# Optimization experiments

Measured on AMD Instinct MI355X. Metric: run time of the kernel, lower is better.

## Reference

```python
import jax, jax.numpy as jnp
import numpy as np

D = 1024
H = 16
DH = D // H
NEG = -10000000.0


def setup_inputs() -> dict:
    key = jax.random.key(0)
    ks = jax.random.split(key, 12)
    B, L = 2, 2048
    sc = 0.02
    inp = {
        "q": jax.random.normal(ks[0], (B, L, D), jnp.float32),
        "k": jax.random.normal(ks[1], (B, L, D), jnp.float32),
        "v": jax.random.normal(ks[2], (B, L, D), jnp.float32),
        "attention_mask": jax.random.randint(ks[3], (B, L, L), 0, 2) == 1,
        "head_mask": jnp.ones((1, 1, 1), jnp.float32),
        "Wq": sc * jax.random.normal(ks[4], (D, D), jnp.float32),
        "bq": jnp.zeros((D,), jnp.float32),
        "Wk": sc * jax.random.normal(ks[5], (D, D), jnp.float32),
        "bk": jnp.zeros((D,), jnp.float32),
        "Wv": sc * jax.random.normal(ks[6], (D, D), jnp.float32),
        "bv": jnp.zeros((D,), jnp.float32),
        "Wo": sc * jax.random.normal(ks[7], (D, D), jnp.float32),
        "bo": jnp.zeros((D,), jnp.float32),
    }
    return inp


def reference(q, k, v, attention_mask, head_mask, Wq, bq, Wk, bk, Wv, bv, Wo, bo):
    B, Lq, _ = q.shape
    Lk = k.shape[1]
    # QKV projections (nn.Linear: x @ W.T + b), split into heads
    qh = (q @ Wq.T + bq).reshape(B, Lq, H, DH)  # [B,Lq,H,dh]
    kh = (k @ Wk.T + bk).reshape(B, Lk, H, DH)
    vh = (v @ Wv.T + bv).reshape(B, Lk, H, DH)
    # scores [B,H,Lq,Lk], scaled by 1/sqrt(dh)
    scores = jnp.einsum("bihd,bjhd->bhij", qh, kh) / jnp.sqrt(jnp.float32(DH))
    scores = jnp.where(attention_mask[:, None, :, :], NEG, scores)
    probs = jax.nn.softmax(scores, axis=-1)
    probs = probs * head_mask  # broadcastable head mask (dropout is identity in eval)
    ctx = jnp.einsum("bhij,bjhd->bihd", probs, vh).reshape(B, Lq, D)
    # output linear + residual (Add_and_LN with with_lN=False, eval dropout)
    out = ctx @ Wo.T + bo + q
    return out
```

## Files before the change

kernel.cpp:

```cpp
#include <hip/hip_runtime.h>

typedef unsigned short u16;
typedef unsigned long long u64;
typedef __attribute__((ext_vector_type(4))) float f32x4;
typedef __attribute__((ext_vector_type(8))) short s16x8;
typedef __attribute__((ext_vector_type(4))) short s16x4;
typedef __attribute__((ext_vector_type(4))) unsigned int u32x4;

#define LDS_LOAD16(gp, lp) __builtin_amdgcn_global_load_lds( \
    (__attribute__((address_space(1))) void*)(gp), \
    (__attribute__((address_space(3))) void*)(lp), 16, 0, 0)

#define MFMA16 __builtin_amdgcn_mfma_f32_16x16x32_bf16

constexpr float L2E = 1.44269504088896340736f;

__device__ __forceinline__ u16 f2bf(float x) {
  unsigned u = __float_as_uint(x);
  u += 0x7FFF + ((u >> 16) & 1);
  return (u16)(u >> 16);
}

__device__ __forceinline__ unsigned cvtpk_bf16(float lo, float hi) {
  unsigned r;
  asm("v_cvt_pk_bf16_f32 %0, %1, %2" : "=v"(r) : "v"(lo), "v"(hi));
  return r;
}

struct PrepArgs {
  const float* src[7];
  u16* dst[7];
  int n4[7];
  float scale[7];
  const unsigned* mask;
  u64* bits;
  int nmask;
  int nconv;
};

__global__ __launch_bounds__(256) void prep_all(PrepArgs a) {
  const int arr = blockIdx.y;
  if (arr == a.nconv) {
    const int lane = threadIdx.x & 63;
    unsigned probe = a.mask[lane];
    bool bytemode = __any(probe > 1u);
    const int stride = gridDim.x * blockDim.x;
    for (int i = blockIdx.x * blockDim.x + threadIdx.x; i < a.nmask; i += stride) {
      bool v;
      if (bytemode) v = ((const unsigned char*)a.mask)[i] != 0;
      else          v = a.mask[i] != 0;
      u64 b = __ballot(v);
      if (lane == 0) a.bits[i >> 6] = b;
    }
    return;
  }
  const f32x4* src = (const f32x4*)a.src[arr];
  u16* dst = a.dst[arr];
  const int n4 = a.n4[arr];
  const float sc = a.scale[arr];
  const int stride = gridDim.x * blockDim.x;
  for (int i = blockIdx.x * blockDim.x + threadIdx.x; i < n4; i += stride) {
    f32x4 v = src[i];
    s16x4 o;
#pragma unroll
    for (int j = 0; j < 4; ++j) o[j] = (short)f2bf(v[j] * sc);
    *(s16x4*)(dst + (size_t)i * 4) = o;
  }
}

struct QkvArgsB {
  const u16* A[3];
  const u16* B[3];
  const float* bias[3];
  float bscale[3];
  u16* C[3];
};

__global__ __launch_bounds__(256) void gemm_qkv_bf(QkvArgsB a) {
  const int z = blockIdx.z;
  const u16* __restrict__ A = a.A[z];
  const u16* __restrict__ B = a.B[z];
  const float* __restrict__ bias = a.bias[z];
  const float bscale = a.bscale[z];
  u16* __restrict__ C = a.C[z];

  __shared__ u16 As[3][4096];
  __shared__ u16 Bs[3][4096];
  const int tid = threadIdx.x;
  const int lane = tid & 63;
  const int wave = tid >> 6;
  const int g = lane >> 4, c = lane & 15;
  const int g4 = g * 4;
  const int bx = blockIdx.x;
  const int row0 = (((bx & 7) << 2) | (bx >> 3)) * 128;
  const int col0 = blockIdx.y * 128;
  const int wr = (wave >> 1) * 64, wc = (wave & 1) * 64;

  f32x4 acc[4][4] = {};

#define STAGE_QKV(p_, k0_) { _Pragma("unroll") \
    for (int i = 0; i < 2; ++i) { \
      int e = (i * 256 + tid) * 8; \
      LDS_LOAD16(A + (size_t)(row0 + (e >> 5)) * 1024 + (k0_) + (e & 31), As[p_] + e); \
      LDS_LOAD16(B + (size_t)(col0 + (e >> 5)) * 1024 + (k0_) + (e & 31), Bs[p_] + e); } }

  STAGE_QKV(0, 0);
  STAGE_QKV(1, 32);

  for (int s = 0; s < 32; ++s) {
    const int p = s % 3;
    if (s == 31) asm volatile("s_waitcnt vmcnt(0)" ::: "memory");
    else         asm volatile("s_waitcnt vmcnt(4)" ::: "memory");
    __builtin_amdgcn_s_barrier();
    __builtin_amdgcn_sched_barrier(0);
    if (s + 2 < 32) {
      const int np = (s + 2) % 3;
      STAGE_QKV(np, (s + 2) * 32);
    }
    s16x8 af[4], bf[4];
#pragma unroll
    for (int m = 0; m < 4; ++m) af[m] = *(const s16x8*)(As[p] + (wr + m * 16 + c) * 32 + g * 8);
#pragma unroll
    for (int n = 0; n < 4; ++n) bf[n] = *(const s16x8*)(Bs[p] + (wc + n * 16 + c) * 32 + g * 8);
#pragma unroll
    for (int m = 0; m < 4; ++m)
#pragma unroll
      for (int n = 0; n < 4; ++n)
        acc[m][n] = MFMA16(bf[n], af[m], acc[m][n], 0, 0, 0);
  }

  f32x4 bv[4];
#pragma unroll
  for (int n = 0; n < 4; ++n) {
    bv[n] = *(const f32x4*)(bias + col0 + wc + n * 16 + g4);
#pragma unroll
    for (int r = 0; r < 4; ++r) bv[n][r] *= bscale;
  }
#pragma unroll
  for (int m = 0; m < 4; ++m)
#pragma unroll
    for (int n = 0; n < 4; ++n) {
      s16x4 o;
#pragma unroll
      for (int r = 0; r < 4; ++r) o[r] = (short)f2bf(acc[m][n][r] + bv[n][r]);
      *(s16x4*)(C + (size_t)(row0 + wr + m * 16 + c) * 1024 + col0 + wc + n * 16 + g4) = o;
    }
}

struct QkvArgsF {
  const float* A[3];
  const u16* B[3];
  const float* bias[3];
  float bscale[3];
  u16* C[3];
};

__global__ __launch_bounds__(256) void gemm_qkv_f32(QkvArgsF a) {
  const int z = blockIdx.z;
  const float* __restrict__ A = a.A[z];
  const u16* __restrict__ B = a.B[z];
  const float* __restrict__ bias = a.bias[z];
  const float bscale = a.bscale[z];
  u16* __restrict__ C = a.C[z];

  __shared__ u16 As[2][4096];
  __shared__ u16 Bs[2][4096];
  const int tid = threadIdx.x;
  const int lane = tid & 63;
  const int wave = tid >> 6;
  const int g = lane >> 4, c = lane & 15;
  const int g4 = g * 4;
  const int row0 = blockIdx.x * 128;
  const int col0 = blockIdx.y * 128;
  const int wr = (wave >> 1) * 64, wc = (wave & 1) * 64;
  const int ra = tid >> 2;
  const int cca = (tid & 3) * 8;

  f32x4 acc[4][4] = {};
  f32x4 ar[2][2];
#pragma unroll
  for (int i = 0; i < 2; ++i) {
    ar[i][0] = *(const f32x4*)(A + (size_t)(row0 + i * 64 + ra) * 1024 + cca);
    ar[i][1] = *(const f32x4*)(A + (size_t)(row0 + i * 64 + ra) * 1024 + cca + 4);
  }

  for (int s = 0; s < 32; ++s) {
    const int p = s & 1;
    const int k0 = s * 32;
#pragma unroll
    for (int i = 0; i < 2; ++i) {
      unsigned w0 = cvtpk_bf16(ar[i][0][0], ar[i][0][1]);
      unsigned w1 = cvtpk_bf16(ar[i][0][2], ar[i][0][3]);
      unsigned w2 = cvtpk_bf16(ar[i][1][0], ar[i][1][1]);
      unsigned w3 = cvtpk_bf16(ar[i][1][2], ar[i][1][3]);
      union { u32x4 u; s16x8 v; } w;
      w.u = (u32x4){w0, w1, w2, w3};
      *(s16x8*)(As[p] + (i * 256 + tid) * 8) = w.v;
    }
    if (s < 31) {
#pragma unroll
      for (int i = 0; i < 2; ++i) {
        ar[i][0] = *(const f32x4*)(A + (size_t)(row0 + i * 64 + ra) * 1024 + k0 + 32 + cca);
        ar[i][1] = *(const f32x4*)(A + (size_t)(row0 + i * 64 + ra) * 1024 + k0 + 32 + cca + 4);
      }
    }
#pragma unroll
    for (int i = 0; i < 2; ++i) {
      int e = (i * 256 + tid) * 8;
      LDS_LOAD16(B + (size_t)(col0 + (e >> 5)) * 1024 + k0 + (e & 31), Bs[p] + e);
    }
    __syncthreads();

    s16x8 af[4], bf[4];
#pragma unroll
    for (int m = 0; m < 4; ++m) af[m] = *(const s16x8*)(As[p] + (wr + m * 16 + c) * 32 + g * 8);
#pragma unroll
    for (int n = 0; n < 4; ++n) bf[n] = *(const s16x8*)(Bs[p] + (wc + n * 16 + c) * 32 + g * 8);
#pragma unroll
    for (int m = 0; m < 4; ++m)
#pragma unroll
      for (int n = 0; n < 4; ++n)
        acc[m][n] = MFMA16(bf[n], af[m], acc[m][n], 0, 0, 0);
  }

  f32x4 bv[4];
#pragma unroll
  for (int n = 0; n < 4; ++n) {
    bv[n] = *(const f32x4*)(bias + col0 + wc + n * 16 + g4);
#pragma unroll
    for (int r = 0; r < 4; ++r) bv[n][r] *= bscale;
  }
#pragma unroll
  for (int m = 0; m < 4; ++m)
#pragma unroll
    for (int n = 0; n < 4; ++n) {
      s16x4 o;
#pragma unroll
      for (int r = 0; r < 4; ++r) o[r] = (short)f2bf(acc[m][n][r] + bv[n][r]);
      *(s16x4*)(C + (size_t)(row0 + wr + m * 16 + c) * 1024 + col0 + wc + n * 16 + g4) = o;
    }
}

__global__ __launch_bounds__(256) void gemm_out(const u16* __restrict__ A,
                                                const u16* __restrict__ B,
                                                const float* __restrict__ bias,
                                                const float* __restrict__ resid,
                                                float* __restrict__ C) {
  __shared__ u16 As[3][2048];
  __shared__ u16 Bs[3][4096];
  const int tid = threadIdx.x;
  const int lane = tid & 63;
  const int wave = tid >> 6;
  const int g = lane >> 4, c = lane & 15;
  const int g4 = g * 4;
  const int bx = blockIdx.x;
  const int row0 = (((bx & 7) << 3) | (bx >> 3)) * 64;
  const int col0 = blockIdx.y * 128;
  const int wr = (wave >> 1) * 32, wc = (wave & 1) * 64;

  f32x4 acc[2][4] = {};

#define STAGE_OUT(p_, k0_) { \
    LDS_LOAD16(A + (size_t)(row0 + (tid >> 2)) * 1024 + (k0_) + (tid & 3) * 8, As[p_] + tid * 8); \
    _Pragma("unroll") \
    for (int i = 0; i < 2; ++i) { \
      int e = (i * 256 + tid) * 8; \
      LDS_LOAD16(B + (size_t)(col0 + (e >> 5)) * 1024 + (k0_) + (e & 31), Bs[p_] + e); } }

  STAGE_OUT(0, 0);
  STAGE_OUT(1, 32);

  for (int s = 0; s < 32; ++s) {
    const int p = s % 3;
    if (s == 31) asm volatile("s_waitcnt vmcnt(0)" ::: "memory");
    else         asm volatile("s_waitcnt vmcnt(3)" ::: "memory");
    __builtin_amdgcn_s_barrier();
    __builtin_amdgcn_sched_barrier(0);
    if (s + 2 < 32) {
      const int np = (s + 2) % 3;
      STAGE_OUT(np, (s + 2) * 32);
    }
    s16x8 af[2], bf[4];
#pragma unroll
    for (int m = 0; m < 2; ++m) af[m] = *(const s16x8*)(As[p] + (wr + m * 16 + c) * 32 + g * 8);
#pragma unroll
    for (int n = 0; n < 4; ++n) bf[n] = *(const s16x8*)(Bs[p] + (wc + n * 16 + c) * 32 + g * 8);
#pragma unroll
    for (int m = 0; m < 2; ++m)
#pragma unroll
      for (int n = 0; n < 4; ++n)
        acc[m][n] = MFMA16(bf[n], af[m], acc[m][n], 0, 0, 0);
  }

  f32x4 bv[4];
#pragma unroll
  for (int n = 0; n < 4; ++n) bv[n] = *(const f32x4*)(bias + col0 + wc + n * 16 + g4);
#pragma unroll
  for (int m = 0; m < 2; ++m)
#pragma unroll
    for (int n = 0; n < 4; ++n) {
      size_t off = (size_t)(row0 + wr + m * 16 + c) * 1024 + col0 + wc + n * 16 + g4;
      f32x4 rv = *(const f32x4*)(resid + off);
      f32x4 o;
#pragma unroll
      for (int r = 0; r < 4; ++r) o[r] = acc[m][n][r] + bv[n][r] + rv[r];
      *(f32x4*)(C + off) = o;
    }
}

constexpr float NEGV = -10000000.0f;

__global__ __launch_bounds__(256) void attn_kernel(const u16* __restrict__ Qh,
                                                   const u16* __restrict__ Kh,
                                                   const u16* __restrict__ Vh,
                                                   const u64* __restrict__ mbits,
                                                   const float* __restrict__ head_mask,
                                                   u16* __restrict__ ctx) {
  __shared__ u16 Ks[2][4096];
  __shared__ u16 Vt[2][64 * 72];

  const int tid = threadIdx.x;
  const int lane = tid & 63;
  const int wave = tid >> 6;
  const int g = lane >> 4, c = lane & 15;
  const int g4 = g * 4;
  const int wid = (blockIdx.x & 7) * 64 + (blockIdx.x >> 3);
  const int qt = wid & 15;
  const int bh = wid >> 4;
  const int b = bh >> 4;
  const int h = bh & 15;
  const size_t rowbase = (size_t)b * 2048;
  const int D = 1024;

  s16x8 qf[2][2];
#pragma unroll
  for (int s = 0; s < 2; ++s) {
    const int qrow = qt * 128 + s * 64 + wave * 16 + c;
#pragma unroll
    for (int ks = 0; ks < 2; ++ks)
      qf[s][ks] = *(const s16x8*)(Qh + (rowbase + qrow) * D + h * 64 + ks * 32 + g * 8);
  }

  f32x4 accO[2][4] = {};
  f32x4 accSum[2] = {};

  union { u32x4 u; s16x8 v; } onesu;
  onesu.u = (u32x4){0x3F803F80u, 0x3F803F80u, 0x3F803F80u, 0x3F803F80u};
  const s16x8 onesA = onesu.v;

  const u64* mrow0 = mbits + (rowbase + qt * 128 + 0 * 64 + wave * 16 + c) * 32;
  const u64* mrow1 = mbits + (rowbase + qt * 128 + 1 * 64 + wave * 16 + c) * 32;

  const int kkK = tid & 63;
  const int aV = tid >> 3;
  const int sV = tid & 7;
  const int dcV = sV * 8;
  const int k2 = 2 * aV;
  const int slotV = (k2 & 32) | (((k2 >> 2) & 3) << 3) | (((k2 >> 4) & 1) << 2) | (k2 & 3);
  const int colV = slotV ^ (8 * sV);

  const u16* Kbase = Kh + rowbase * D + h * 64;
  const u16* Vbase = Vh + rowbase * D + h * 64;

  s16x8 kreg[2], vreg[2];
#define LOADKV(kb_) { \
    kreg[0] = *(const s16x8*)(Kbase + (size_t)((kb_) + kkK) * D + wave * 8); \
    kreg[1] = *(const s16x8*)(Kbase + (size_t)((kb_) + kkK) * D + (4 + wave) * 8); \
    vreg[0] = *(const s16x8*)(Vbase + (size_t)((kb_) + k2) * D + dcV); \
    vreg[1] = *(const s16x8*)(Vbase + (size_t)((kb_) + k2 + 1) * D + dcV); }
#define WRITEKV(p_) { \
    *(s16x8*)(Ks[p_] + tid * 8) = kreg[0]; \
    *(s16x8*)(Ks[p_] + 2048 + tid * 8) = kreg[1]; \
    const unsigned* v0w = (const unsigned*)&vreg[0]; \
    const unsigned* v1w = (const unsigned*)&vreg[1]; \
    _Pragma("unroll") \
    for (int j = 0; j < 8; ++j) { \
      unsigned pk = __builtin_amdgcn_perm(v1w[j >> 1], v0w[j >> 1], \
                                          (j & 1) ? 0x07060302u : 0x05040100u); \
      *(unsigned*)(Vt[p_] + (dcV + j) * 72 + colV) = pk; } }

  LOADKV(0);
  WRITEKV(0);
  LOADKV(64);
  __syncthreads();

#define ATTN_ITER(p_, it_) { \
    const int it = (it_); \
    if (it < 31) WRITEKV(p_ ^ 1); \
    if (it < 30) LOADKV((it + 2) * 64); \
    f32x4 accS[2][4]; \
    _Pragma("unroll") \
    for (int t = 0; t < 4; ++t) { \
      s16x8 kf0 = *(const s16x8*)(Ks[p_] + ((0 + g) * 64 + t * 16 + c) * 8); \
      s16x8 kf1 = *(const s16x8*)(Ks[p_] + ((4 + g) * 64 + t * 16 + c) * 8); \
      f32x4 z0 = {0.f, 0.f, 0.f, 0.f}; \
      z0 = MFMA16(kf0, qf[0][0], z0, 0, 0, 0); \
      accS[0][t] = MFMA16(kf1, qf[0][1], z0, 0, 0, 0); \
      f32x4 z1 = {0.f, 0.f, 0.f, 0.f}; \
      z1 = MFMA16(kf0, qf[1][0], z1, 0, 0, 0); \
      accS[1][t] = MFMA16(kf1, qf[1][1], z1, 0, 0, 0); \
    } \
    s16x8 vbr[4][2]; \
    _Pragma("unroll") \
    for (int d0 = 0; d0 < 4; ++d0) { \
      const int dd = d0 * 16 + c; \
      const int sw8 = (d0 * 2 + (c >> 3)) * 8; \
      _Pragma("unroll") \
      for (int ks = 0; ks < 2; ++ks) \
        vbr[d0][ks] = *(const s16x8*)(Vt[p_] + dd * 72 + ((ks * 32 + g * 8) ^ sw8)); \
    } \
    s16x8 pa[2][2]; \
    _Pragma("unroll") \
    for (int s = 0; s < 2; ++s) { \
      u64 mw = (s == 0 ? mrow0 : mrow1)[it]; \
      u64 sh = mw >> g4; \
      unsigned mlo = (unsigned)sh, mhi = (unsigned)(sh >> 32); \
      unsigned pk0[4], pk1[4]; \
      _Pragma("unroll") \
      for (int t = 0; t < 4; ++t) { \
        unsigned msrc = (t < 2) ? mlo : mhi; \
        _Pragma("unroll") \
        for (int r = 0; r < 4; ++r) { \
          float sv = accS[s][t][r]; \
          if ((msrc >> ((t & 1) * 16 + r)) & 1) sv = NEGV; \
          float pv; \
          asm("v_exp_f32 %0, %1" : "=v"(pv) : "v"(sv)); \
          accS[s][t][r] = pv; \
        } \
        pk0[t] = cvtpk_bf16(accS[s][t][0], accS[s][t][1]); \
        pk1[t] = cvtpk_bf16(accS[s][t][2], accS[s][t][3]); \
      } \
      _Pragma("unroll") \
      for (int ks = 0; ks < 2; ++ks) { \
        union { u32x4 u; s16x8 v; } w; \
        w.u = (u32x4){pk0[2 * ks], pk1[2 * ks], pk0[2 * ks + 1], pk1[2 * ks + 1]}; \
        pa[s][ks] = w.v; \
      } \
    } \
    _Pragma("unroll") \
    for (int d0 = 0; d0 < 4; ++d0) \
      _Pragma("unroll") \
      for (int ks = 0; ks < 2; ++ks) { \
        accO[0][d0] = MFMA16(vbr[d0][ks], pa[0][ks], accO[0][d0], 0, 0, 0); \
        accO[1][d0] = MFMA16(vbr[d0][ks], pa[1][ks], accO[1][d0], 0, 0, 0); \
      } \
    _Pragma("unroll") \
    for (int ks = 0; ks < 2; ++ks) { \
      accSum[0] = MFMA16(onesA, pa[0][ks], accSum[0], 0, 0, 0); \
      accSum[1] = MFMA16(onesA, pa[1][ks], accSum[1], 0, 0, 0); \
    } \
    __syncthreads(); }

  for (int it2 = 0; it2 < 16; ++it2) {
    ATTN_ITER(0, 2 * it2);
    ATTN_ITER(1, 2 * it2 + 1);
  }

  const float hm = head_mask[0];
#pragma unroll
  for (int s = 0; s < 2; ++s) {
    float inv = hm / accSum[s][0];
    const int qrow = qt * 128 + s * 64 + wave * 16 + c;
#pragma unroll
    for (int d0 = 0; d0 < 4; ++d0) {
      s16x4 o;
#pragma unroll
      for (int r = 0; r < 4; ++r) o[r] = (short)f2bf(accO[s][d0][r] * inv);
      *(s16x4*)(ctx + (rowbase + qrow) * D + h * 64 + d0 * 16 + g4) = o;
    }
  }
}

extern "C" void kernel_launch(void* const* d_in, const int* in_sizes, int n_in,
                              void* d_out, int out_size, void* d_ws, size_t ws_size,
                              hipStream_t stream) {
  const float* q  = (const float*)d_in[0];
  const float* k  = (const float*)d_in[1];
  const float* v  = (const float*)d_in[2];
  const void*  am = d_in[3];
  const float* hm = (const float*)d_in[4];
  const float* Wq = (const float*)d_in[5];
  const float* bq = (const float*)d_in[6];
  const float* Wk = (const float*)d_in[7];
  const float* bk = (const float*)d_in[8];
  const float* Wv = (const float*)d_in[9];
  const float* bv = (const float*)d_in[10];
  const float* Wo = (const float*)d_in[11];
  const float* bo = (const float*)d_in[12];

  char* ws = (char*)d_ws;
  const size_t MB = 1024 * 1024;
  const bool big = ws_size >= 58 * MB;

  if (big) {
    u16* qb  = (u16*)(ws + 0 * MB);
    u16* kb  = (u16*)(ws + 8 * MB);
    u16* vb  = (u16*)(ws + 16 * MB);
    u16* wqb = (u16*)(ws + 24 * MB);
    u16* wkb = (u16*)(ws + 26 * MB);
    u16* wvb = (u16*)(ws + 28 * MB);
    u16* wob = (u16*)(ws + 30 * MB);
    u16* Qh  = (u16*)(ws + 32 * MB);
    u16* Kh  = (u16*)(ws + 40 * MB);
    u16* Vh  = (u16*)(ws + 48 * MB);
    u64* mbits = (u64*)(ws + 56 * MB);
    u16* ctx = qb;

    PrepArgs ca;
    ca.src[0] = q;  ca.dst[0] = qb;  ca.n4[0] = 1048576; ca.scale[0] = 1.f;
    ca.src[1] = k;  ca.dst[1] = kb;  ca.n4[1] = 1048576; ca.scale[1] = 1.f;
    ca.src[2] = v;  ca.dst[2] = vb;  ca.n4[2] = 1048576; ca.scale[2] = 1.f;
    ca.src[3] = Wq; ca.dst[3] = wqb; ca.n4[3] = 262144;  ca.scale[3] = 0.125f * L2E;
    ca.src[4] = Wk; ca.dst[4] = wkb; ca.n4[4] = 262144;  ca.scale[4] = 1.f;
    ca.src[5] = Wv; ca.dst[5] = wvb; ca.n4[5] = 262144;  ca.scale[5] = 1.f;
    ca.src[6] = Wo; ca.dst[6] = wob; ca.n4[6] = 262144;  ca.scale[6] = 1.f;
    ca.mask = (const unsigned*)am; ca.bits = mbits; ca.nmask = 8388608; ca.nconv = 7;
    prep_all<<<dim3(512, 8), 256, 0, stream>>>(ca);

    QkvArgsB ga;
    ga.A[0] = qb; ga.B[0] = wqb; ga.bias[0] = bq; ga.bscale[0] = 0.125f * L2E; ga.C[0] = Qh;
    ga.A[1] = kb; ga.B[1] = wkb; ga.bias[1] = bk; ga.bscale[1] = 1.f;          ga.C[1] = Kh;
    ga.A[2] = vb; ga.B[2] = wvb; ga.bias[2] = bv; ga.bscale[2] = 1.f;          ga.C[2] = Vh;
    gemm_qkv_bf<<<dim3(32, 8, 3), 256, 0, stream>>>(ga);

    attn_kernel<<<512, 256, 0, stream>>>(Qh, Kh, Vh, mbits, hm, ctx);

    gemm_out<<<dim3(64, 8), 256, 0, stream>>>(ctx, wob, bo, q, (float*)d_out);
  } else {
    u16* Qh  = (u16*)(ws + 0 * MB);
    u16* Kh  = (u16*)(ws + 8 * MB);
    u16* Vh  = (u16*)(ws + 16 * MB);
    u16* wqb = (u16*)(ws + 24 * MB);
    u16* wkb = (u16*)(ws + 26 * MB);
    u16* wvb = (u16*)(ws + 28 * MB);
    u16* wob = (u16*)(ws + 30 * MB);
    u64* mbits = (u64*)(ws + 32 * MB);
    u16* ctx = (u16*)(ws + 33 * MB);

    PrepArgs ca;
    ca.src[0] = Wq; ca.dst[0] = wqb; ca.n4[0] = 262144; ca.scale[0] = 0.125f * L2E;
    ca.src[1] = Wk; ca.dst[1] = wkb; ca.n4[1] = 262144; ca.scale[1] = 1.f;
    ca.src[2] = Wv; ca.dst[2] = wvb; ca.n4[2] = 262144; ca.scale[2] = 1.f;
    ca.src[3] = Wo; ca.dst[3] = wob; ca.n4[3] = 262144; ca.scale[3] = 1.f;
    ca.mask = (const unsigned*)am; ca.bits = mbits; ca.nmask = 8388608; ca.nconv = 4;
    prep_all<<<dim3(512, 5), 256, 0, stream>>>(ca);

    QkvArgsF ga;
    ga.A[0] = q; ga.B[0] = wqb; ga.bias[0] = bq; ga.bscale[0] = 0.125f * L2E; ga.C[0] = Qh;
    ga.A[1] = k; ga.B[1] = wkb; ga.bias[1] = bk; ga.bscale[1] = 1.f;          ga.C[1] = Kh;
    ga.A[2] = v; ga.B[2] = wvb; ga.bias[2] = bv; ga.bscale[2] = 1.f;          ga.C[2] = Vh;
    gemm_qkv_f32<<<dim3(32, 8, 3), 256, 0, stream>>>(ga);

    attn_kernel<<<512, 256, 0, stream>>>(Qh, Kh, Vh, mbits, hm, ctx);

    gemm_out<<<dim3(64, 8), 256, 0, stream>>>(ctx, wob, bo, q, (float*)d_out);
  }
}
```

Measured before the change: 164.9 us.

## Halve attention query tile to 64 rows and split mask prep kernel

The attention kernel now gives each block 64 query rows instead of 128, doubling the grid to 1024 blocks and adding a launch-bounds hint of 4 blocks per CU for occupancy. Fewer accumulators per thread lowers register pressure, but each K/V tile loaded into LDS is now reused by half as many queries, so K/V traffic doubles. The mask-to-bitmask conversion is also split out of the fused prep kernel into its own launch, which adds one kernel launch.

```diff
diff --git a/kernel.cpp b/kernel.cpp
--- a/kernel.cpp
+++ b/kernel.cpp
@@ -27,33 +27,15 @@
   return r;
 }
 
-struct PrepArgs {
+struct ConvArgs {
   const float* src[7];
   u16* dst[7];
   int n4[7];
   float scale[7];
-  const unsigned* mask;
-  u64* bits;
-  int nmask;
-  int nconv;
 };
 
-__global__ __launch_bounds__(256) void prep_all(PrepArgs a) {
+__global__ __launch_bounds__(256) void convert_many(ConvArgs a) {
   const int arr = blockIdx.y;
-  if (arr == a.nconv) {
-    const int lane = threadIdx.x & 63;
-    unsigned probe = a.mask[lane];
-    bool bytemode = __any(probe > 1u);
-    const int stride = gridDim.x * blockDim.x;
-    for (int i = blockIdx.x * blockDim.x + threadIdx.x; i < a.nmask; i += stride) {
-      bool v;
-      if (bytemode) v = ((const unsigned char*)a.mask)[i] != 0;
-      else          v = a.mask[i] != 0;
-      u64 b = __ballot(v);
-      if (lane == 0) a.bits[i >> 6] = b;
-    }
-    return;
-  }
   const f32x4* src = (const f32x4*)a.src[arr];
   u16* dst = a.dst[arr];
   const int n4 = a.n4[arr];
@@ -65,6 +47,22 @@
 #pragma unroll
     for (int j = 0; j < 4; ++j) o[j] = (short)f2bf(v[j] * sc);
     *(s16x4*)(dst + (size_t)i * 4) = o;
+  }
+}
+
+__global__ __launch_bounds__(256) void mask_to_bits(const unsigned int* __restrict__ m32,
+                                                    u64* __restrict__ bits,
+                                                    int n) {
+  const int lane = threadIdx.x & 63;
+  unsigned probe = m32[lane];
+  bool bytemode = __any(probe > 1u);
+  const int stride = gridDim.x * blockDim.x;
+  for (int i = blockIdx.x * blockDim.x + threadIdx.x; i < n; i += stride) {
+    bool v;
+    if (bytemode) v = ((const unsigned char*)m32)[i] != 0;
+    else          v = m32[i] != 0;
+    u64 b = __ballot(v);
+    if (lane == 0) bits[i >> 6] = b;
   }
 }
 
@@ -310,12 +308,12 @@
 
 constexpr float NEGV = -10000000.0f;
 
-__global__ __launch_bounds__(256) void attn_kernel(const u16* __restrict__ Qh,
-                                                   const u16* __restrict__ Kh,
-                                                   const u16* __restrict__ Vh,
-                                                   const u64* __restrict__ mbits,
-                                                   const float* __restrict__ head_mask,
-                                                   u16* __restrict__ ctx) {
+__global__ __launch_bounds__(256, 4) void attn_kernel(const u16* __restrict__ Qh,
+                                                      const u16* __restrict__ Kh,
+                                                      const u16* __restrict__ Vh,
+                                                      const u64* __restrict__ mbits,
+                                                      const float* __restrict__ head_mask,
+                                                      u16* __restrict__ ctx) {
   __shared__ u16 Ks[2][4096];
   __shared__ u16 Vt[2][64 * 72];
 
@@ -324,32 +322,28 @@
   const int wave = tid >> 6;
   const int g = lane >> 4, c = lane & 15;
   const int g4 = g * 4;
-  const int wid = (blockIdx.x & 7) * 64 + (blockIdx.x >> 3);
-  const int qt = wid & 15;
-  const int bh = wid >> 4;
+  const int wid = (blockIdx.x & 7) * 128 + (blockIdx.x >> 3);
+  const int qt = wid & 31;
+  const int bh = wid >> 5;
   const int b = bh >> 4;
   const int h = bh & 15;
   const size_t rowbase = (size_t)b * 2048;
   const int D = 1024;
 
-  s16x8 qf[2][2];
-#pragma unroll
-  for (int s = 0; s < 2; ++s) {
-    const int qrow = qt * 128 + s * 64 + wave * 16 + c;
-#pragma unroll
-    for (int ks = 0; ks < 2; ++ks)
-      qf[s][ks] = *(const s16x8*)(Qh + (rowbase + qrow) * D + h * 64 + ks * 32 + g * 8);
-  }
-
-  f32x4 accO[2][4] = {};
-  f32x4 accSum[2] = {};
+  const int qrow = qt * 64 + wave * 16 + c;
+  s16x8 qf[2];
+#pragma unroll
+  for (int ks = 0; ks < 2; ++ks)
+    qf[ks] = *(const s16x8*)(Qh + (rowbase + qrow) * D + h * 64 + ks * 32 + g * 8);
+
+  f32x4 accO[4] = {};
+  f32x4 accSum = {};
 
   union { u32x4 u; s16x8 v; } onesu;
   onesu.u = (u32x4){0x3F803F80u, 0x3F803F80u, 0x3F803F80u, 0x3F803F80u};
   const s16x8 onesA = onesu.v;
 
-  const u64* mrow0 = mbits + (rowbase + qt * 128 + 0 * 64 + wave * 16 + c) * 32;
-  const u64* mrow1 = mbits + (rowbase + qt * 128 + 1 * 64 + wave * 16 + c) * 32;
+  const u64* mrow = mbits + (rowbase + qrow) * 32;
 
   const int kkK = tid & 63;
   const int aV = tid >> 3;
@@ -388,17 +382,14 @@
     const int it = (it_); \
     if (it < 31) WRITEKV(p_ ^ 1); \
     if (it < 30) LOADKV((it + 2) * 64); \
-    f32x4 accS[2][4]; \
+    f32x4 accS[4]; \
     _Pragma("unroll") \
     for (int t = 0; t < 4; ++t) { \
       s16x8 kf0 = *(const s16x8*)(Ks[p_] + ((0 + g) * 64 + t * 16 + c) * 8); \
       s16x8 kf1 = *(const s16x8*)(Ks[p_] + ((4 + g) * 64 + t * 16 + c) * 8); \
-      f32x4 z0 = {0.f, 0.f, 0.f, 0.f}; \
-      z0 = MFMA16(kf0, qf[0][0], z0, 0, 0, 0); \
-      accS[0][t] = MFMA16(kf1, qf[0][1], z0, 0, 0, 0); \
-      f32x4 z1 = {0.f, 0.f, 0.f, 0.f}; \
-      z1 = MFMA16(kf0, qf[1][0], z1, 0, 0, 0); \
-      accS[1][t] = MFMA16(kf1, qf[1][1], z1, 0, 0, 0); \
+      f32x4 z = {0.f, 0.f, 0.f, 0.f}; \
+      z = MFMA16(kf0, qf[0], z, 0, 0, 0); \
+      accS[t] = MFMA16(kf1, qf[1], z, 0, 0, 0); \
     } \
     s16x8 vbr[4][2]; \
     _Pragma("unroll") \
@@ -409,46 +400,39 @@
       for (int ks = 0; ks < 2; ++ks) \
         vbr[d0][ks] = *(const s16x8*)(Vt[p_] + dd * 72 + ((ks * 32 + g * 8) ^ sw8)); \
     } \
-    s16x8 pa[2][2]; \
-    _Pragma("unroll") \
-    for (int s = 0; s < 2; ++s) { \
-      u64 mw = (s == 0 ? mrow0 : mrow1)[it]; \
-      u64 sh = mw >> g4; \
-      unsigned mlo = (unsigned)sh, mhi = (unsigned)(sh >> 32); \
-      unsigned pk0[4], pk1[4]; \
+    u64 mw = mrow[it]; \
+    u64 sh = mw >> g4; \
+    unsigned mlo = (unsigned)sh, mhi = (unsigned)(sh >> 32); \
+    unsigned pk0[4], pk1[4]; \
+    _Pragma("unroll") \
+    for (int t = 0; t < 4; ++t) { \
+      unsigned msrc = (t < 2) ? mlo : mhi; \
       _Pragma("unroll") \
-      for (int t = 0; t < 4; ++t) { \
-        unsigned msrc = (t < 2) ? mlo : mhi; \
-        _Pragma("unroll") \
-        for (int r = 0; r < 4; ++r) { \
-          float sv = accS[s][t][r]; \
-          if ((msrc >> ((t & 1) * 16 + r)) & 1) sv = NEGV; \
-          float pv; \
-          asm("v_exp_f32 %0, %1" : "=v"(pv) : "v"(sv)); \
-          accS[s][t][r] = pv; \
-        } \
-        pk0[t] = cvtpk_bf16(accS[s][t][0], accS[s][t][1]); \
-        pk1[t] = cvtpk_bf16(accS[s][t][2], accS[s][t][3]); \
+      for (int r = 0; r < 4; ++r) { \
+        float sv = accS[t][r]; \
+        if ((msrc >> ((t & 1) * 16 + r)) & 1) sv = NEGV; \
+        float pv; \
+        asm("v_exp_f32 %0, %1" : "=v"(pv) : "v"(sv)); \
+        accS[t][r] = pv; \
       } \
-      _Pragma("unroll") \
-      for (int ks = 0; ks < 2; ++ks) { \
-        union { u32x4 u; s16x8 v; } w; \
-        w.u = (u32x4){pk0[2 * ks], pk1[2 * ks], pk0[2 * ks + 1], pk1[2 * ks + 1]}; \
-        pa[s][ks] = w.v; \
-      } \
+      pk0[t] = cvtpk_bf16(accS[t][0], accS[t][1]); \
+      pk1[t] = cvtpk_bf16(accS[t][2], accS[t][3]); \
+    } \
+    s16x8 pa[2]; \
+    _Pragma("unroll") \
+    for (int ks = 0; ks < 2; ++ks) { \
+      union { u32x4 u; s16x8 v; } w; \
+      w.u = (u32x4){pk0[2 * ks], pk1[2 * ks], pk0[2 * ks + 1], pk1[2 * ks + 1]}; \
+      pa[ks] = w.v; \
     } \
     _Pragma("unroll") \
     for (int d0 = 0; d0 < 4; ++d0) \
       _Pragma("unroll") \
-      for (int ks = 0; ks < 2; ++ks) { \
-        accO[0][d0] = MFMA16(vbr[d0][ks], pa[0][ks], accO[0][d0], 0, 0, 0); \
-        accO[1][d0] = MFMA16(vbr[d0][ks], pa[1][ks], accO[1][d0], 0, 0, 0); \
-      } \
-    _Pragma("unroll") \
-    for (int ks = 0; ks < 2; ++ks) { \
-      accSum[0] = MFMA16(onesA, pa[0][ks], accSum[0], 0, 0, 0); \
-      accSum[1] = MFMA16(onesA, pa[1][ks], accSum[1], 0, 0, 0); \
-    } \
+      for (int ks = 0; ks < 2; ++ks) \
+        accO[d0] = MFMA16(vbr[d0][ks], pa[ks], accO[d0], 0, 0, 0); \
+    _Pragma("unroll") \
+    for (int ks = 0; ks < 2; ++ks) \
+      accSum = MFMA16(onesA, pa[ks], accSum, 0, 0, 0); \
     __syncthreads(); }
 
   for (int it2 = 0; it2 < 16; ++it2) {
@@ -457,17 +441,13 @@
   }
 
   const float hm = head_mask[0];
-#pragma unroll
-  for (int s = 0; s < 2; ++s) {
-    float inv = hm / accSum[s][0];
-    const int qrow = qt * 128 + s * 64 + wave * 16 + c;
-#pragma unroll
-    for (int d0 = 0; d0 < 4; ++d0) {
-      s16x4 o;
-#pragma unroll
-      for (int r = 0; r < 4; ++r) o[r] = (short)f2bf(accO[s][d0][r] * inv);
-      *(s16x4*)(ctx + (rowbase + qrow) * D + h * 64 + d0 * 16 + g4) = o;
-    }
+  float inv = hm / accSum[0];
+#pragma unroll
+  for (int d0 = 0; d0 < 4; ++d0) {
+    s16x4 o;
+#pragma unroll
+    for (int r = 0; r < 4; ++r) o[r] = (short)f2bf(accO[d0][r] * inv);
+    *(s16x4*)(ctx + (rowbase + qrow) * D + h * 64 + d0 * 16 + g4) = o;
   }
 }
 
@@ -506,7 +486,7 @@
     u64* mbits = (u64*)(ws + 56 * MB);
     u16* ctx = qb;
 
-    PrepArgs ca;
+    ConvArgs ca;
     ca.src[0] = q;  ca.dst[0] = qb;  ca.n4[0] = 1048576; ca.scale[0] = 1.f;
     ca.src[1] = k;  ca.dst[1] = kb;  ca.n4[1] = 1048576; ca.scale[1] = 1.f;
     ca.src[2] = v;  ca.dst[2] = vb;  ca.n4[2] = 1048576; ca.scale[2] = 1.f;
@@ -514,8 +494,9 @@
     ca.src[4] = Wk; ca.dst[4] = wkb; ca.n4[4] = 262144;  ca.scale[4] = 1.f;
     ca.src[5] = Wv; ca.dst[5] = wvb; ca.n4[5] = 262144;  ca.scale[5] = 1.f;
     ca.src[6] = Wo; ca.dst[6] = wob; ca.n4[6] = 262144;  ca.scale[6] = 1.f;
-    ca.mask = (const unsigned*)am; ca.bits = mbits; ca.nmask = 8388608; ca.nconv = 7;
-    prep_all<<<dim3(512, 8), 256, 0, stream>>>(ca);
+    convert_many<<<dim3(512, 7), 256, 0, stream>>>(ca);
+
+    mask_to_bits<<<2048, 256, 0, stream>>>((const unsigned int*)am, mbits, 8388608);
 
     QkvArgsB ga;
     ga.A[0] = qb; ga.B[0] = wqb; ga.bias[0] = bq; ga.bscale[0] = 0.125f * L2E; ga.C[0] = Qh;
@@ -523,7 +504,7 @@
     ga.A[2] = vb; ga.B[2] = wvb; ga.bias[2] = bv; ga.bscale[2] = 1.f;          ga.C[2] = Vh;
     gemm_qkv_bf<<<dim3(32, 8, 3), 256, 0, stream>>>(ga);
 
-    attn_kernel<<<512, 256, 0, stream>>>(Qh, Kh, Vh, mbits, hm, ctx);
+    attn_kernel<<<1024, 256, 0, stream>>>(Qh, Kh, Vh, mbits, hm, ctx);
 
     gemm_out<<<dim3(64, 8), 256, 0, stream>>>(ctx, wob, bo, q, (float*)d_out);
   } else {
@@ -537,13 +518,14 @@
     u64* mbits = (u64*)(ws + 32 * MB);
     u16* ctx = (u16*)(ws + 33 * MB);
 
-    PrepArgs ca;
+    ConvArgs ca;
     ca.src[0] = Wq; ca.dst[0] = wqb; ca.n4[0] = 262144; ca.scale[0] = 0.125f * L2E;
     ca.src[1] = Wk; ca.dst[1] = wkb; ca.n4[1] = 262144; ca.scale[1] = 1.f;
     ca.src[2] = Wv; ca.dst[2] = wvb; ca.n4[2] = 262144; ca.scale[2] = 1.f;
     ca.src[3] = Wo; ca.dst[3] = wob; ca.n4[3] = 262144; ca.scale[3] = 1.f;
-    ca.mask = (const unsigned*)am; ca.bits = mbits; ca.nmask = 8388608; ca.nconv = 4;
-    prep_all<<<dim3(512, 5), 256, 0, stream>>>(ca);
+    convert_many<<<dim3(256, 4), 256, 0, stream>>>(ca);
+
+    mask_to_bits<<<2048, 256, 0, stream>>>((const unsigned int*)am, mbits, 8388608);
 
     QkvArgsF ga;
     ga.A[0] = q; ga.B[0] = wqb; ga.bias[0] = bq; ga.bscale[0] = 0.125f * L2E; ga.C[0] = Qh;
@@ -551,7 +533,7 @@
     ga.A[2] = v; ga.B[2] = wvb; ga.bias[2] = bv; ga.bscale[2] = 1.f;          ga.C[2] = Vh;
     gemm_qkv_f32<<<dim3(32, 8, 3), 256, 0, stream>>>(ga);
 
-    attn_kernel<<<512, 256, 0, stream>>>(Qh, Kh, Vh, mbits, hm, ctx);
+    attn_kernel<<<1024, 256, 0, stream>>>(Qh, Kh, Vh, mbits, hm, ctx);
 
     gemm_out<<<dim3(64, 8), 256, 0, stream>>>(ctx, wob, bo, q, (float*)d_out);
   }
```

After: 151.5 us. 8.1% less time.

## Split attention over key halves with a combine pass; separate mask kernel

Applied to the files above, without the earlier changes.

Attention now runs 1024 blocks, each covering half of the key sequence. Each block writes unnormalized bf16 partial outputs and row sums, and a new combine kernel adds the halves and normalizes. The goal is more parallelism and better CU occupancy, helped by launch_bounds(256,4). The mask-to-bits conversion moves out of the fused prep kernel into its own launch. This costs an extra kernel launch plus a round trip through global memory for the partials, and rounding the partials to bf16 loses some precision.

```diff
diff --git a/kernel.cpp b/kernel.cpp
--- a/kernel.cpp
+++ b/kernel.cpp
@@ -21,39 +21,25 @@
   return (u16)(u >> 16);
 }
 
+__device__ __forceinline__ float bf2f(u16 x) {
+  return __uint_as_float(((unsigned)x) << 16);
+}
+
 __device__ __forceinline__ unsigned cvtpk_bf16(float lo, float hi) {
   unsigned r;
   asm("v_cvt_pk_bf16_f32 %0, %1, %2" : "=v"(r) : "v"(lo), "v"(hi));
   return r;
 }
 
-struct PrepArgs {
+struct ConvArgs {
   const float* src[7];
   u16* dst[7];
   int n4[7];
   float scale[7];
-  const unsigned* mask;
-  u64* bits;
-  int nmask;
-  int nconv;
 };
 
-__global__ __launch_bounds__(256) void prep_all(PrepArgs a) {
+__global__ __launch_bounds__(256) void convert_many(ConvArgs a) {
   const int arr = blockIdx.y;
-  if (arr == a.nconv) {
-    const int lane = threadIdx.x & 63;
-    unsigned probe = a.mask[lane];
-    bool bytemode = __any(probe > 1u);
-    const int stride = gridDim.x * blockDim.x;
-    for (int i = blockIdx.x * blockDim.x + threadIdx.x; i < a.nmask; i += stride) {
-      bool v;
-      if (bytemode) v = ((const unsigned char*)a.mask)[i] != 0;
-      else          v = a.mask[i] != 0;
-      u64 b = __ballot(v);
-      if (lane == 0) a.bits[i >> 6] = b;
-    }
-    return;
-  }
   const f32x4* src = (const f32x4*)a.src[arr];
   u16* dst = a.dst[arr];
   const int n4 = a.n4[arr];
@@ -65,6 +51,22 @@
 #pragma unroll
     for (int j = 0; j < 4; ++j) o[j] = (short)f2bf(v[j] * sc);
     *(s16x4*)(dst + (size_t)i * 4) = o;
+  }
+}
+
+__global__ __launch_bounds__(256) void mask_to_bits(const unsigned int* __restrict__ m32,
+                                                    u64* __restrict__ bits,
+                                                    int n) {
+  const int lane = threadIdx.x & 63;
+  unsigned probe = m32[lane];
+  bool bytemode = __any(probe > 1u);
+  const int stride = gridDim.x * blockDim.x;
+  for (int i = blockIdx.x * blockDim.x + threadIdx.x; i < n; i += stride) {
+    bool v;
+    if (bytemode) v = ((const unsigned char*)m32)[i] != 0;
+    else          v = m32[i] != 0;
+    u64 b = __ballot(v);
+    if (lane == 0) bits[i >> 6] = b;
   }
 }
 
@@ -310,12 +312,16 @@
 
 constexpr float NEGV = -10000000.0f;
 
-__global__ __launch_bounds__(256) void attn_kernel(const u16* __restrict__ Qh,
-                                                   const u16* __restrict__ Kh,
-                                                   const u16* __restrict__ Vh,
-                                                   const u64* __restrict__ mbits,
-                                                   const float* __restrict__ head_mask,
-                                                   u16* __restrict__ ctx) {
+__global__ __launch_bounds__(256, 4) void attn_kernel(const u16* __restrict__ Qh,
+                                                      const u16* __restrict__ Kh,
+                                                      const u16* __restrict__ Vh,
+                                                      const u64* __restrict__ mbits,
+                                                      const float* __restrict__ head_mask,
+                                                      u16* __restrict__ O0,
+                                                      u16* __restrict__ O1,
+                                                      float* __restrict__ s0p,
+                                                      float* __restrict__ s1p,
+                                                      int niter) {
   __shared__ u16 Ks[2][4096];
   __shared__ u16 Vt[2][64 * 72];
 
@@ -324,13 +330,18 @@
   const int wave = tid >> 6;
   const int g = lane >> 4, c = lane & 15;
   const int g4 = g * 4;
-  const int wid = (blockIdx.x & 7) * 64 + (blockIdx.x >> 3);
+  const int nb = gridDim.x >> 3;
+  const int wid = (blockIdx.x & 7) * nb + (blockIdx.x >> 3);
   const int qt = wid & 15;
-  const int bh = wid >> 4;
+  const int rest = wid >> 4;
+  const int bh = rest & 31;
+  const int half = rest >> 5;
   const int b = bh >> 4;
   const int h = bh & 15;
   const size_t rowbase = (size_t)b * 2048;
   const int D = 1024;
+  const int kb0 = half * niter * 64;
+  const int mbase = half * niter;
 
   s16x8 qf[2][2];
 #pragma unroll
@@ -379,15 +390,15 @@
                                           (j & 1) ? 0x07060302u : 0x05040100u); \
       *(unsigned*)(Vt[p_] + (dcV + j) * 72 + colV) = pk; } }
 
-  LOADKV(0);
+  LOADKV(kb0);
   WRITEKV(0);
-  LOADKV(64);
+  LOADKV(kb0 + 64);
   __syncthreads();
 
 #define ATTN_ITER(p_, it_) { \
     const int it = (it_); \
-    if (it < 31) WRITEKV(p_ ^ 1); \
-    if (it < 30) LOADKV((it + 2) * 64); \
+    if (it < niter - 1) WRITEKV(p_ ^ 1); \
+    if (it < niter - 2) LOADKV(kb0 + (it + 2) * 64); \
     f32x4 accS[2][4]; \
     _Pragma("unroll") \
     for (int t = 0; t < 4; ++t) { \
@@ -412,7 +423,7 @@
     s16x8 pa[2][2]; \
     _Pragma("unroll") \
     for (int s = 0; s < 2; ++s) { \
-      u64 mw = (s == 0 ? mrow0 : mrow1)[it]; \
+      u64 mw = (s == 0 ? mrow0 : mrow1)[mbase + it]; \
       u64 sh = mw >> g4; \
       unsigned mlo = (unsigned)sh, mhi = (unsigned)(sh >> 32); \
       unsigned pk0[4], pk1[4]; \
@@ -451,23 +462,65 @@
     } \
     __syncthreads(); }
 
-  for (int it2 = 0; it2 < 16; ++it2) {
+  const int n2 = niter >> 1;
+  for (int it2 = 0; it2 < n2; ++it2) {
     ATTN_ITER(0, 2 * it2);
     ATTN_ITER(1, 2 * it2 + 1);
   }
 
-  const float hm = head_mask[0];
-#pragma unroll
-  for (int s = 0; s < 2; ++s) {
-    float inv = hm / accSum[s][0];
-    const int qrow = qt * 128 + s * 64 + wave * 16 + c;
-#pragma unroll
-    for (int d0 = 0; d0 < 4; ++d0) {
-      s16x4 o;
-#pragma unroll
-      for (int r = 0; r < 4; ++r) o[r] = (short)f2bf(accO[s][d0][r] * inv);
-      *(s16x4*)(ctx + (rowbase + qrow) * D + h * 64 + d0 * 16 + g4) = o;
-    }
+  if (s0p) {
+    u16* outp = half ? O1 : O0;
+    float* sp = half ? s1p : s0p;
+#pragma unroll
+    for (int s = 0; s < 2; ++s) {
+      const int qrow = qt * 128 + s * 64 + wave * 16 + c;
+      if (g == 0) sp[(rowbase + qrow) * 16 + h] = accSum[s][0];
+#pragma unroll
+      for (int d0 = 0; d0 < 4; ++d0) {
+        s16x4 o;
+#pragma unroll
+        for (int r = 0; r < 4; ++r) o[r] = (short)f2bf(accO[s][d0][r]);
+        *(s16x4*)(outp + (rowbase + qrow) * D + h * 64 + d0 * 16 + g4) = o;
+      }
+    }
+  } else {
+    const float hm = head_mask[0];
+#pragma unroll
+    for (int s = 0; s < 2; ++s) {
+      float inv = hm / accSum[s][0];
+      const int qrow = qt * 128 + s * 64 + wave * 16 + c;
+#pragma unroll
+      for (int d0 = 0; d0 < 4; ++d0) {
+        s16x4 o;
+#pragma unroll
+        for (int r = 0; r < 4; ++r) o[r] = (short)f2bf(accO[s][d0][r] * inv);
+        *(s16x4*)(O0 + (rowbase + qrow) * D + h * 64 + d0 * 16 + g4) = o;
+      }
+    }
+  }
+}
+
+__global__ __launch_bounds__(256) void combine_halves(const u16* __restrict__ O0,
+                                                      const u16* __restrict__ O1,
+                                                      const float* __restrict__ s0,
+                                                      const float* __restrict__ s1,
+                                                      const float* __restrict__ hm,
+                                                      u16* __restrict__ ctx) {
+  const float hmv = hm[0];
+  const int stride = gridDim.x * blockDim.x;
+  for (int i = blockIdx.x * blockDim.x + threadIdx.x; i < 524288; i += stride) {
+    const int e = i * 8;
+    const int row = e >> 10;
+    const int h = (e >> 6) & 15;
+    const int sidx = row * 16 + h;
+    const float inv = hmv / (s0[sidx] + s1[sidx]);
+    s16x8 a = *(const s16x8*)(O0 + e);
+    s16x8 bb = *(const s16x8*)(O1 + e);
+    s16x8 o;
+#pragma unroll
+    for (int j = 0; j < 8; ++j)
+      o[j] = (short)f2bf((bf2f((u16)a[j]) + bf2f((u16)bb[j])) * inv);
+    *(s16x8*)(ctx + e) = o;
   }
 }
 
@@ -504,9 +557,11 @@
     u16* Kh  = (u16*)(ws + 40 * MB);
     u16* Vh  = (u16*)(ws + 48 * MB);
     u64* mbits = (u64*)(ws + 56 * MB);
+    float* sums0 = (float*)(ws + 57 * MB);
+    float* sums1 = (float*)(ws + 57 * MB + 262144);
     u16* ctx = qb;
 
-    PrepArgs ca;
+    ConvArgs ca;
     ca.src[0] = q;  ca.dst[0] = qb;  ca.n4[0] = 1048576; ca.scale[0] = 1.f;
     ca.src[1] = k;  ca.dst[1] = kb;  ca.n4[1] = 1048576; ca.scale[1] = 1.f;
     ca.src[2] = v;  ca.dst[2] = vb;  ca.n4[2] = 1048576; ca.scale[2] = 1.f;
@@ -514,8 +569,9 @@
     ca.src[4] = Wk; ca.dst[4] = wkb; ca.n4[4] = 262144;  ca.scale[4] = 1.f;
     ca.src[5] = Wv; ca.dst[5] = wvb; ca.n4[5] = 262144;  ca.scale[5] = 1.f;
     ca.src[6] = Wo; ca.dst[6] = wob; ca.n4[6] = 262144;  ca.scale[6] = 1.f;
-    ca.mask = (const unsigned*)am; ca.bits = mbits; ca.nmask = 8388608; ca.nconv = 7;
-    prep_all<<<dim3(512, 8), 256, 0, stream>>>(ca);
+    convert_many<<<dim3(512, 7), 256, 0, stream>>>(ca);
+
+    mask_to_bits<<<2048, 256, 0, stream>>>((const unsigned int*)am, mbits, 8388608);
 
     QkvArgsB ga;
     ga.A[0] = qb; ga.B[0] = wqb; ga.bias[0] = bq; ga.bscale[0] = 0.125f * L2E; ga.C[0] = Qh;
@@ -523,7 +579,9 @@
     ga.A[2] = vb; ga.B[2] = wvb; ga.bias[2] = bv; ga.bscale[2] = 1.f;          ga.C[2] = Vh;
     gemm_qkv_bf<<<dim3(32, 8, 3), 256, 0, stream>>>(ga);
 
-    attn_kernel<<<512, 256, 0, stream>>>(Qh, Kh, Vh, mbits, hm, ctx);
+    attn_kernel<<<1024, 256, 0, stream>>>(Qh, Kh, Vh, mbits, hm,
+                                          kb, vb, sums0, sums1, 16);
+    combine_halves<<<2048, 256, 0, stream>>>(kb, vb, sums0, sums1, hm, ctx);
 
     gemm_out<<<dim3(64, 8), 256, 0, stream>>>(ctx, wob, bo, q, (float*)d_out);
   } else {
@@ -537,13 +595,14 @@
     u64* mbits = (u64*)(ws + 32 * MB);
     u16* ctx = (u16*)(ws + 33 * MB);
 
-    PrepArgs ca;
+    ConvArgs ca;
     ca.src[0] = Wq; ca.dst[0] = wqb; ca.n4[0] = 262144; ca.scale[0] = 0.125f * L2E;
     ca.src[1] = Wk; ca.dst[1] = wkb; ca.n4[1] = 262144; ca.scale[1] = 1.f;
     ca.src[2] = Wv; ca.dst[2] = wvb; ca.n4[2] = 262144; ca.scale[2] = 1.f;
     ca.src[3] = Wo; ca.dst[3] = wob; ca.n4[3] = 262144; ca.scale[3] = 1.f;
-    ca.mask = (const unsigned*)am; ca.bits = mbits; ca.nmask = 8388608; ca.nconv = 4;
-    prep_all<<<dim3(512, 5), 256, 0, stream>>>(ca);
+    convert_many<<<dim3(256, 4), 256, 0, stream>>>(ca);
+
+    mask_to_bits<<<2048, 256, 0, stream>>>((const unsigned int*)am, mbits, 8388608);
 
     QkvArgsF ga;
     ga.A[0] = q; ga.B[0] = wqb; ga.bias[0] = bq; ga.bscale[0] = 0.125f * L2E; ga.C[0] = Qh;
@@ -551,7 +610,8 @@
     ga.A[2] = v; ga.B[2] = wvb; ga.bias[2] = bv; ga.bscale[2] = 1.f;          ga.C[2] = Vh;
     gemm_qkv_f32<<<dim3(32, 8, 3), 256, 0, stream>>>(ga);
 
-    attn_kernel<<<512, 256, 0, stream>>>(Qh, Kh, Vh, mbits, hm, ctx);
+    attn_kernel<<<512, 256, 0, stream>>>(Qh, Kh, Vh, mbits, hm,
+                                         ctx, nullptr, nullptr, nullptr, 32);
 
     gemm_out<<<dim3(64, 8), 256, 0, stream>>>(ctx, wob, bo, q, (float*)d_out);
   }
```

Result: slower. 176.3 us (+6.9%).

## Move mask bit-packing into QKV GEMM launch to overlap with matmul

Applied to the files above, without the earlier changes.

On the large-workspace path, the attention-mask-to-bitmask conversion moves out of the prep kernel and into an extra z-slice of the QKV GEMM grid. The memory-bound mask pass then runs alongside the compute-bound GEMM blocks instead of beside the conversion work, which is also memory-bound. The small-workspace path splits mask packing into its own kernel launch, which adds a launch there. Risks are an extra slice of 256 blocks in the GEMM grid and weaker overlap if the mask blocks are scheduled last.

```diff
diff --git a/kernel.cpp b/kernel.cpp
--- a/kernel.cpp
+++ b/kernel.cpp
@@ -27,33 +27,15 @@
   return r;
 }
 
-struct PrepArgs {
+struct ConvArgs {
   const float* src[7];
   u16* dst[7];
   int n4[7];
   float scale[7];
-  const unsigned* mask;
-  u64* bits;
-  int nmask;
-  int nconv;
 };
 
-__global__ __launch_bounds__(256) void prep_all(PrepArgs a) {
+__global__ __launch_bounds__(256) void convert_many(ConvArgs a) {
   const int arr = blockIdx.y;
-  if (arr == a.nconv) {
-    const int lane = threadIdx.x & 63;
-    unsigned probe = a.mask[lane];
-    bool bytemode = __any(probe > 1u);
-    const int stride = gridDim.x * blockDim.x;
-    for (int i = blockIdx.x * blockDim.x + threadIdx.x; i < a.nmask; i += stride) {
-      bool v;
-      if (bytemode) v = ((const unsigned char*)a.mask)[i] != 0;
-      else          v = a.mask[i] != 0;
-      u64 b = __ballot(v);
-      if (lane == 0) a.bits[i >> 6] = b;
-    }
-    return;
-  }
   const f32x4* src = (const f32x4*)a.src[arr];
   u16* dst = a.dst[arr];
   const int n4 = a.n4[arr];
@@ -68,16 +50,51 @@
   }
 }
 
+__global__ __launch_bounds__(256) void mask_to_bits(const unsigned int* __restrict__ m32,
+                                                    u64* __restrict__ bits,
+                                                    int n) {
+  const int lane = threadIdx.x & 63;
+  unsigned probe = m32[lane];
+  bool bytemode = __any(probe > 1u);
+  const int stride = gridDim.x * blockDim.x;
+  for (int i = blockIdx.x * blockDim.x + threadIdx.x; i < n; i += stride) {
+    bool v;
+    if (bytemode) v = ((const unsigned char*)m32)[i] != 0;
+    else          v = m32[i] != 0;
+    u64 b = __ballot(v);
+    if (lane == 0) bits[i >> 6] = b;
+  }
+}
+
 struct QkvArgsB {
   const u16* A[3];
   const u16* B[3];
   const float* bias[3];
   float bscale[3];
   u16* C[3];
+  const unsigned* mask;
+  u64* bits;
+  int nmask;
 };
 
 __global__ __launch_bounds__(256) void gemm_qkv_bf(QkvArgsB a) {
   const int z = blockIdx.z;
+  if (z == 3) {
+    const int lane = threadIdx.x & 63;
+    unsigned probe = a.mask[lane];
+    bool bytemode = __any(probe > 1u);
+    const int nb = gridDim.x * gridDim.y;
+    const int bid = blockIdx.y * gridDim.x + blockIdx.x;
+    const int stride = nb * blockDim.x;
+    for (int i = bid * blockDim.x + threadIdx.x; i < a.nmask; i += stride) {
+      bool v;
+      if (bytemode) v = ((const unsigned char*)a.mask)[i] != 0;
+      else          v = a.mask[i] != 0;
+      u64 b = __ballot(v);
+      if (lane == 0) a.bits[i >> 6] = b;
+    }
+    return;
+  }
   const u16* __restrict__ A = a.A[z];
   const u16* __restrict__ B = a.B[z];
   const float* __restrict__ bias = a.bias[z];
@@ -506,7 +523,7 @@
     u64* mbits = (u64*)(ws + 56 * MB);
     u16* ctx = qb;
 
-    PrepArgs ca;
+    ConvArgs ca;
     ca.src[0] = q;  ca.dst[0] = qb;  ca.n4[0] = 1048576; ca.scale[0] = 1.f;
     ca.src[1] = k;  ca.dst[1] = kb;  ca.n4[1] = 1048576; ca.scale[1] = 1.f;
     ca.src[2] = v;  ca.dst[2] = vb;  ca.n4[2] = 1048576; ca.scale[2] = 1.f;
@@ -514,14 +531,14 @@
     ca.src[4] = Wk; ca.dst[4] = wkb; ca.n4[4] = 262144;  ca.scale[4] = 1.f;
     ca.src[5] = Wv; ca.dst[5] = wvb; ca.n4[5] = 262144;  ca.scale[5] = 1.f;
     ca.src[6] = Wo; ca.dst[6] = wob; ca.n4[6] = 262144;  ca.scale[6] = 1.f;
-    ca.mask = (const unsigned*)am; ca.bits = mbits; ca.nmask = 8388608; ca.nconv = 7;
-    prep_all<<<dim3(512, 8), 256, 0, stream>>>(ca);
+    convert_many<<<dim3(512, 7), 256, 0, stream>>>(ca);
 
     QkvArgsB ga;
     ga.A[0] = qb; ga.B[0] = wqb; ga.bias[0] = bq; ga.bscale[0] = 0.125f * L2E; ga.C[0] = Qh;
     ga.A[1] = kb; ga.B[1] = wkb; ga.bias[1] = bk; ga.bscale[1] = 1.f;          ga.C[1] = Kh;
     ga.A[2] = vb; ga.B[2] = wvb; ga.bias[2] = bv; ga.bscale[2] = 1.f;          ga.C[2] = Vh;
-    gemm_qkv_bf<<<dim3(32, 8, 3), 256, 0, stream>>>(ga);
+    ga.mask = (const unsigned*)am; ga.bits = mbits; ga.nmask = 8388608;
+    gemm_qkv_bf<<<dim3(32, 8, 4), 256, 0, stream>>>(ga);
 
     attn_kernel<<<512, 256, 0, stream>>>(Qh, Kh, Vh, mbits, hm, ctx);
 
@@ -537,13 +554,14 @@
     u64* mbits = (u64*)(ws + 32 * MB);
     u16* ctx = (u16*)(ws + 33 * MB);
 
-    PrepArgs ca;
+    ConvArgs ca;
     ca.src[0] = Wq; ca.dst[0] = wqb; ca.n4[0] = 262144; ca.scale[0] = 0.125f * L2E;
     ca.src[1] = Wk; ca.dst[1] = wkb; ca.n4[1] = 262144; ca.scale[1] = 1.f;
     ca.src[2] = Wv; ca.dst[2] = wvb; ca.n4[2] = 262144; ca.scale[2] = 1.f;
     ca.src[3] = Wo; ca.dst[3] = wob; ca.n4[3] = 262144; ca.scale[3] = 1.f;
-    ca.mask = (const unsigned*)am; ca.bits = mbits; ca.nmask = 8388608; ca.nconv = 4;
-    prep_all<<<dim3(512, 5), 256, 0, stream>>>(ca);
+    convert_many<<<dim3(256, 4), 256, 0, stream>>>(ca);
+
+    mask_to_bits<<<2048, 256, 0, stream>>>((const unsigned int*)am, mbits, 8388608);
 
     QkvArgsF ga;
     ga.A[0] = q; ga.B[0] = wqb; ga.bias[0] = bq; ga.bscale[0] = 0.125f * L2E; ga.C[0] = Qh;
```

New measurement: 179.6 us. +8.9%, slower.
